# Kernel tuning notes

Measured on AMD Instinct MI355X. Metric: run time of the kernel, lower is better.

The kernel has to match this reference:

```python
import jax, jax.numpy as jnp
import numpy as np
import math

DIM = 256
PATCH = 16  # Patchnum
H = W = 64  # feature_size
B = 16


def _conv(x, w, pad):
    # x: [B,C,H,W], w: [O,I,kh,kw]
    return jax.lax.conv_general_dilated(
        x, w, window_strides=(1, 1), padding=[(pad, pad), (pad, pad)],
        dimension_numbers=('NCHW', 'OIHW', 'NCHW'))


def setup_inputs() -> dict:
    key = jax.random.key(0)
    ks = jax.random.split(key, 6)
    fan = DIM * 9
    s3 = 1.0 / math.sqrt(fan)
    s1 = 1.0 / math.sqrt(DIM)
    return {
        'e': jax.random.normal(ks[0], (B, DIM, H, W), dtype=jnp.float32),
        'pam_out': jax.random.normal(ks[1], (B, DIM, PATCH, PATCH), dtype=jnp.float32),
        'q_w': jax.random.uniform(ks[2], (DIM, DIM, 3, 3), jnp.float32, -s3, s3),
        'k_w': jax.random.uniform(ks[3], (DIM, DIM, 3, 3), jnp.float32, -s3, s3),
        'v_w': jax.random.uniform(ks[4], (DIM, DIM, 3, 3), jnp.float32, -s3, s3),
        'proj_w': jax.random.uniform(ks[5], (DIM, DIM, 1, 1), jnp.float32, -s1, s1),
    }


def reference(e, pam_out, q_w, k_w, v_w, proj_w):
    b, c, h, w = e.shape
    # AdaptiveAvgPool2d((PATCH, PATCH)) with h % PATCH == 0 -> mean pooling
    fh, fw = h // PATCH, w // PATCH
    max_e = e.reshape(b, c, PATCH, fh, PATCH, fw).mean(axis=(3, 5))
    q = _conv(max_e, q_w, 1).reshape(b, c, PATCH * PATCH)      # [b,c,P^2]
    k = _conv(pam_out, k_w, 1).reshape(b, c, PATCH * PATCH)    # [b,c,P^2]
    v = _conv(e, v_w, 1).reshape(b, c, h * w)                  # [b,c,HW]
    # L2 normalize along token dim (torch F.normalize, eps=1e-12)
    q = q / jnp.maximum(jnp.linalg.norm(q, axis=-1, keepdims=True), 1e-12)
    k = k / jnp.maximum(jnp.linalg.norm(k, axis=-1, keepdims=True), 1e-12)
    attn = jnp.einsum('bcn,bdn->bcd', q, k) / math.sqrt(c)     # [b,c,c]
    attn = jax.nn.softmax(attn, axis=-1)
    out = jnp.einsum('bcd,bdn->bcn', attn, v).reshape(b, c, h, w)
    out = _conv(out, proj_w, 0) + e
    return out
```

## Files before the change

kernel.cpp:

```cpp
#include <hip/hip_runtime.h>
#include <hip/hip_bf16.h>

#define NB 16
#define NC 256
#define NPIX 4096

typedef __attribute__((ext_vector_type(8))) short short8;
typedef __attribute__((ext_vector_type(4))) short short4v;
typedef __attribute__((ext_vector_type(4))) float f32x4;

static __device__ __forceinline__ ushort f2bf(float f) {
    __hip_bfloat16 h = __float2bfloat16(f);
    return *(ushort*)&h;
}

static __device__ __forceinline__ void gload_lds16(const ushort* g, ushort* l) {
    __builtin_amdgcn_global_load_lds(
        (const __attribute__((address_space(1))) unsigned int*)g,
        (__attribute__((address_space(3))) unsigned int*)l, 16, 0, 0);
}

__global__ void __launch_bounds__(256) prep_k(
    const float* __restrict__ e, const float* __restrict__ pam,
    const float* __restrict__ qw, const float* __restrict__ kw,
    const float* __restrict__ vw, const float* __restrict__ pw,
    ushort* __restrict__ et, ushort* __restrict__ maxeT, ushort* __restrict__ pamT,
    ushort* __restrict__ wqT, ushort* __restrict__ wkT,
    ushort* __restrict__ pbf, ushort* __restrict__ vwT,
    float* __restrict__ qnorm, float* __restrict__ knorm) {
    __shared__ float smem[9216];
    int blk = blockIdx.x, t = threadIdx.x;
    if (blk < 512) {
        int b = blk >> 5;
        int py = (blk >> 1) & 15;
        int xh = blk & 1;
        float (*lt)[32] = (float(*)[32])smem;
        float pool[8];
#pragma unroll
        for (int rr = 0; rr < 8; ++rr) pool[rr] = 0.f;
        int px = t & 7;
        int x4 = px * 4;
        int cg = t >> 3;
        for (int r = 0; r < 4; ++r) {
            int y = py * 4 + r;
            if (r) __syncthreads();
            const float* ep = e + (size_t)b * NC * NPIX + y * 64 + xh * 32;
#pragma unroll
            for (int rr = 0; rr < 8; ++rr) {
                int c = rr * 32 + cg;
                float4 v = *(const float4*)(ep + (size_t)c * NPIX + x4);
                pool[rr] += v.x + v.y + v.z + v.w;
                int s = (c >> 3) & 31;
                lt[c][(x4 + 0) ^ s] = v.x;
                lt[c][(x4 + 1) ^ s] = v.y;
                lt[c][(x4 + 2) ^ s] = v.z;
                lt[c][(x4 + 3) ^ s] = v.w;
            }
            __syncthreads();
            int l = t & 31, c0 = l * 8;
            ushort* op = et + ((size_t)((b * 64 + y) * 64) + xh * 32) * 256;
#pragma unroll
            for (int rx = 0; rx < 4; ++rx) {
                int x = rx * 8 + (t >> 5);
                short8 v;
#pragma unroll
                for (int k = 0; k < 8; ++k) v[k] = (short)f2bf(lt[c0 + k][x ^ l]);
                *(short8*)(op + (size_t)x * 256 + c0) = v;
            }
        }
        int tok = py * 16 + xh * 8 + px;
        ushort* md = maxeT + (size_t)b * 65536 + (size_t)tok * 256;
#pragma unroll
        for (int rr = 0; rr < 8; ++rr)
            md[rr * 32 + cg] = f2bf(pool[rr] * 0.0625f);
    } else if (blk < 768) {
        int bb = blk - 512;
        int b = bb >> 4, cg = bb & 15;
        float (*lt)[256] = (float(*)[256])smem;
#pragma unroll
        for (int cc = 0; cc < 16; ++cc)
            lt[cc][t] = pam[(size_t)(b * 256 + cg * 16 + cc) * 256 + t];
        __syncthreads();
        ushort* dstb = pamT + (size_t)b * 65536 + (size_t)t * 256 + cg * 16;
#pragma unroll
        for (int g = 0; g < 2; ++g) {
            short8 v;
#pragma unroll
            for (int k = 0; k < 8; ++k) v[k] = (short)f2bf(lt[g * 8 + k][t]);
            *(short8*)(dstb + g * 8) = v;
        }
    } else if (blk < 1280) {
        int idx = blk - 768;
        const float* src = (idx < 256) ? qw : kw;
        ushort* dst = (idx < 256) ? wqT : wkT;
        int o = idx & 255;
        float wv[9];
#pragma unroll
        for (int j = 0; j < 9; ++j) wv[j] = src[(size_t)o * 2304 + t * 9 + j];
#pragma unroll
        for (int j = 0; j < 9; ++j) dst[(size_t)j * 65536 + (size_t)o * 256 + t] = f2bf(wv[j]);
    } else if (blk < 1296) {
        int base = (blk - 1280) * 4096;
        for (int g = 0; g < 16; ++g) {
            int idx = base + g * 256 + t;
            pbf[idx] = f2bf(pw[idx]);
        }
    } else if (blk < 1360) {
        int d0 = (blk - 1296) * 4;
        float* lt = smem;
        for (int u = 0; u < 36; ++u) lt[u * 256 + t] = vw[(size_t)d0 * 2304 + u * 256 + t];
        __syncthreads();
#pragma unroll
        for (int r = 0; r < 9; ++r) {
            int idx = r * 256 + t;
            int i = idx / 9, j = idx % 9;
            short4v v;
#pragma unroll
            for (int dd = 0; dd < 4; ++dd) v[dd] = (short)f2bf(lt[dd * 2304 + idx]);
            *(short4v*)(vwT + ((size_t)(j * 256 + i)) * 256 + d0) = v;
        }
    } else {
        for (int g = 0; g < 16; ++g) {
            qnorm[g * 256 + t] = 0.f;
            knorm[g * 256 + t] = 0.f;
        }
    }
}

__global__ void __launch_bounds__(256, 2) conv16_mfma(const ushort* __restrict__ maxeT,
                                                      const ushort* __restrict__ pamT,
                                                      const ushort* __restrict__ wqT,
                                                      const ushort* __restrict__ wkT,
                                                      ushort* __restrict__ qb,
                                                      ushort* __restrict__ kTb,
                                                      float* __restrict__ qnorm,
                                                      float* __restrict__ knorm) {
    int blk = blockIdx.x;
    int qk = blk >> 8;
    int b  = (blk >> 4) & 15;
    int og = (blk >> 2) & 3;
    int tg = blk & 3;
    const ushort* inT = qk ? pamT : maxeT;
    const ushort* wt  = qk ? wkT : wqT;
    ushort* outp      = qk ? kTb : qb;
    float* nrm        = qk ? knorm : qnorm;
    int tid = threadIdx.x, wid = tid >> 6, lane = tid & 63;
    int wm = wid >> 1, wn = wid & 1;
    int kq = lane >> 4, l16 = lane & 15;
    int ty0 = tg * 4;
    __shared__ ushort Bs[96][256];
    __shared__ ushort As[2][64][128];
    const ushort* itb = inT + (size_t)b * 65536;
    {
#pragma unroll
        for (int j = 0; j < 12; ++j) {
            int d = (j * 4 + wid) * 64 + lane;
            int tok = d >> 5, u = d & 31;
            int lr = tok >> 4, tx = tok & 15;
            int gy = min(max(ty0 - 1 + lr, 0), 15);
            gload_lds16(itb + (gy * 16 + tx) * 256 + ((u ^ (tok & 7)) * 8),
                        &Bs[0][0] + (size_t)(j * 4 + wid) * 512);
        }
    }
    int aoff[4];
#pragma unroll
    for (int j = 0; j < 4; ++j) {
        int d = (j * 4 + wid) * 64 + lane;
        int o = d >> 4, u = d & 15;
        aoff[j] = (og * 64 + o) * 256 + ((u ^ (o & 7)) * 8);
    }
    auto stageA = [&](int s, int buf) {
        const ushort* base = wt + (size_t)(s >> 1) * 65536 + (s & 1) * 128;
#pragma unroll
        for (int j = 0; j < 4; ++j)
            gload_lds16(base + aoff[j], &As[buf][0][0] + (size_t)(j * 4 + wid) * 512);
    };
    stageA(0, 0);
    stageA(1, 1);
    __syncthreads();
    f32x4 acc[2][2];
#pragma unroll
    for (int mf = 0; mf < 2; ++mf)
#pragma unroll
        for (int nf = 0; nf < 2; ++nf) acc[mf][nf] = (f32x4){0.f, 0.f, 0.f, 0.f};
    const short8 zf = {};
#pragma unroll
    for (int s = 0; s < 18; ++s) {
        int tap = s >> 1, half = s & 1;
        int dy = tap / 3 - 1, dx = tap % 3 - 1;
        const ushort* bp[2]; bool ok[2]; int lt7[2];
#pragma unroll
        for (int nf = 0; nf < 2; ++nf) {
            int n = tg * 64 + wn * 32 + nf * 16 + l16;
            int ny = (n >> 4) + dy, nx = (n & 15) + dx;
            ok[nf] = ((unsigned)ny < 16u) && ((unsigned)nx < 16u);
            int lrc = min(max(ny - ty0 + 1, 0), 5);
            int nxc = min(max(nx, 0), 15);
            int ltok = lrc * 16 + nxc;
            bp[nf] = &Bs[ltok][0];
            lt7[nf] = ltok & 7;
        }
#pragma unroll
        for (int kc = 0; kc < 4; ++kc) {
            int ua = kc * 4 + kq;
            int ub = half * 16 + kc * 4 + kq;
            short8 af[2], bfr[2];
#pragma unroll
            for (int mf = 0; mf < 2; ++mf) {
                int o = wm * 32 + mf * 16 + l16;
                af[mf] = *(const short8*)(&As[s & 1][o][(ua ^ (o & 7)) * 8]);
            }
#pragma unroll
            for (int nf = 0; nf < 2; ++nf) {
                short8 v = *(const short8*)(bp[nf] + ((ub ^ lt7[nf]) * 8));
                bfr[nf] = ok[nf] ? v : zf;
            }
#pragma unroll
            for (int mf = 0; mf < 2; ++mf)
#pragma unroll
                for (int nf = 0; nf < 2; ++nf)
                    acc[mf][nf] = __builtin_amdgcn_mfma_f32_16x16x32_bf16(af[mf], bfr[nf], acc[mf][nf], 0, 0, 0);
        }
        __syncthreads();
        if (s + 2 < 18) stageA(s + 2, s & 1);
    }
    float ss[2][4];
#pragma unroll
    for (int mf = 0; mf < 2; ++mf)
#pragma unroll
        for (int r = 0; r < 4; ++r) ss[mf][r] = 0.f;
#pragma unroll
    for (int mf = 0; mf < 2; ++mf)
#pragma unroll
        for (int nf = 0; nf < 2; ++nf)
#pragma unroll
            for (int r = 0; r < 4; ++r) ss[mf][r] += acc[mf][nf][r] * acc[mf][nf][r];
#pragma unroll
    for (int mf = 0; mf < 2; ++mf)
#pragma unroll
        for (int r = 0; r < 4; ++r) {
#pragma unroll
            for (int off = 1; off < 16; off <<= 1) ss[mf][r] += __shfl_xor(ss[mf][r], off, 64);
        }
    if (l16 == 0) {
#pragma unroll
        for (int mf = 0; mf < 2; ++mf)
#pragma unroll
            for (int r = 0; r < 4; ++r)
                atomicAdd(&nrm[b * 256 + og * 64 + wm * 32 + mf * 16 + kq * 4 + r], ss[mf][r]);
    }
    ushort* ob = outp + (size_t)b * 65536;
#pragma unroll
    for (int mf = 0; mf < 2; ++mf)
#pragma unroll
        for (int nf = 0; nf < 2; ++nf) {
            int col = tg * 64 + wn * 32 + nf * 16 + l16;
#pragma unroll
            for (int r = 0; r < 4; ++r) {
                int row = og * 64 + wm * 32 + mf * 16 + kq * 4 + r;
                ob[(size_t)row * 256 + col] = f2bf(acc[mf][nf][r]);
            }
        }
}

__global__ void __launch_bounds__(512) attn_mfma(const ushort* __restrict__ qb,
                                                 const ushort* __restrict__ kTb,
                                                 const float* __restrict__ qnorm,
                                                 const float* __restrict__ knorm,
                                                 ushort* __restrict__ attnT) {
    int blk = blockIdx.x;
    int b = (blk & 7) + 8 * ((blk >> 3) & 1);
    int cg = blk >> 4;
    int tid = threadIdx.x, wid = tid >> 6, lane = tid & 63;
    int rw = wid & 1, chf = wid >> 1;
    int kq = lane >> 4, l16 = lane & 15;
    int c0w = cg * 32 + rw * 16;
    int lrow = rw * 16 + kq * 4;
    f32x4 acc[4];
#pragma unroll
    for (int nf = 0; nf < 4; ++nf) acc[nf] = (f32x4){0.f, 0.f, 0.f, 0.f};
    const ushort* qp = qb + (size_t)b * 65536;
    const ushort* kp = kTb + (size_t)b * 65536 + (size_t)(chf * 64) * 256;
    for (int kc = 0; kc < 8; ++kc) {
        short8 af = *(const short8*)(qp + (size_t)(c0w + l16) * 256 + kc * 32 + kq * 8);
#pragma unroll
        for (int nf = 0; nf < 4; ++nf) {
            short8 bf = *(const short8*)(kp + (size_t)(nf * 16 + l16) * 256 + kc * 32 + kq * 8);
            acc[nf] = __builtin_amdgcn_mfma_f32_16x16x32_bf16(af, bf, acc[nf], 0, 0, 0);
        }
    }
    float rq[4], rk[4];
#pragma unroll
    for (int r = 0; r < 4; ++r)
        rq[r] = rsqrtf(fmaxf(qnorm[b * 256 + c0w + kq * 4 + r], 1e-24f)) * 0.0625f;
#pragma unroll
    for (int nf = 0; nf < 4; ++nf)
        rk[nf] = rsqrtf(fmaxf(knorm[b * 256 + chf * 64 + nf * 16 + l16], 1e-24f));
#pragma unroll
    for (int nf = 0; nf < 4; ++nf)
#pragma unroll
        for (int r = 0; r < 4; ++r) acc[nf][r] *= rq[r] * rk[nf];
    __shared__ float red[32][4];
    float m4[4], s4[4];
#pragma unroll
    for (int r = 0; r < 4; ++r) {
        float m = -1e30f;
#pragma unroll
        for (int nf = 0; nf < 4; ++nf) m = fmaxf(m, acc[nf][r]);
#pragma unroll
        for (int off = 1; off < 16; off <<= 1) m = fmaxf(m, __shfl_xor(m, off, 64));
        m4[r] = m;
    }
    if (l16 == 0) {
#pragma unroll
        for (int r = 0; r < 4; ++r) red[lrow + r][chf] = m4[r];
    }
    __syncthreads();
#pragma unroll
    for (int r = 0; r < 4; ++r)
        m4[r] = fmaxf(fmaxf(red[lrow + r][0], red[lrow + r][1]),
                      fmaxf(red[lrow + r][2], red[lrow + r][3]));
    __syncthreads();
#pragma unroll
    for (int r = 0; r < 4; ++r) {
        float s = 0.f;
#pragma unroll
        for (int nf = 0; nf < 4; ++nf) {
            float ex = __expf(acc[nf][r] - m4[r]);
            acc[nf][r] = ex;
            s += ex;
        }
#pragma unroll
        for (int off = 1; off < 16; off <<= 1) s += __shfl_xor(s, off, 64);
        s4[r] = s;
    }
    if (l16 == 0) {
#pragma unroll
        for (int r = 0; r < 4; ++r) red[lrow + r][chf] = s4[r];
    }
    __syncthreads();
#pragma unroll
    for (int r = 0; r < 4; ++r) {
        float inv = 1.0f / (red[lrow + r][0] + red[lrow + r][1] +
                            red[lrow + r][2] + red[lrow + r][3]);
#pragma unroll
        for (int nf = 0; nf < 4; ++nf) acc[nf][r] *= inv;
    }
    ushort* ap = attnT + (size_t)b * 65536;
#pragma unroll
    for (int nf = 0; nf < 4; ++nf) {
        int d = chf * 64 + nf * 16 + l16;
        short4v v;
#pragma unroll
        for (int r = 0; r < 4; ++r) v[r] = (short)f2bf(acc[nf][r]);
        *(short4v*)(ap + (size_t)d * 256 + c0w + kq * 4) = v;
    }
}

__global__ void __launch_bounds__(512) mproj_mfma(const ushort* __restrict__ pbf,
                                                  const ushort* __restrict__ attnT,
                                                  ushort* __restrict__ Mbf) {
    int blk = blockIdx.x;
    int b = (blk & 7) + 8 * ((blk >> 3) & 1);
    int og = blk >> 4;
    int tid = threadIdx.x, wid = tid >> 6, lane = tid & 63;
    int rw = wid & 1, chf = wid >> 1;
    int kq = lane >> 4, l16 = lane & 15;
    int o0w = og * 32 + rw * 16;
    f32x4 acc[4];
#pragma unroll
    for (int nf = 0; nf < 4; ++nf) acc[nf] = (f32x4){0.f, 0.f, 0.f, 0.f};
    const ushort* ap = attnT + (size_t)b * 65536 + (size_t)(chf * 64) * 256;
    for (int kc = 0; kc < 8; ++kc) {
        short8 af = *(const short8*)(pbf + (size_t)(o0w + l16) * 256 + kc * 32 + kq * 8);
#pragma unroll
        for (int nf = 0; nf < 4; ++nf) {
            short8 bf = *(const short8*)(ap + (size_t)(nf * 16 + l16) * 256 + kc * 32 + kq * 8);
            acc[nf] = __builtin_amdgcn_mfma_f32_16x16x32_bf16(af, bf, acc[nf], 0, 0, 0);
        }
    }
    ushort* mb = Mbf + (size_t)b * 65536;
#pragma unroll
    for (int nf = 0; nf < 4; ++nf)
#pragma unroll
        for (int r = 0; r < 4; ++r)
            mb[(size_t)(o0w + kq * 4 + r) * 256 + chf * 64 + nf * 16 + l16] = f2bf(acc[nf][r]);
}

__global__ void __launch_bounds__(512) weff_mfma(const ushort* __restrict__ Mbf,
                                                 const ushort* __restrict__ vwT,
                                                 ushort* __restrict__ wbf) {
    int blk = blockIdx.x;
    int wg = (blk % 8) * 18 + blk / 8;
    int b = wg / 9, j = wg % 9;
    int tid = threadIdx.x;
    int wid = tid >> 6, lane = tid & 63;
    int wm = wid >> 1, wn = wid & 1;
    int kq = lane >> 4, l16 = lane & 15;
    f32x4 acc[4][8];
#pragma unroll
    for (int mf = 0; mf < 4; ++mf)
#pragma unroll
        for (int nf = 0; nf < 8; ++nf) acc[mf][nf] = (f32x4){0.f, 0.f, 0.f, 0.f};
    const ushort* abase = Mbf + (size_t)b * 65536 + (size_t)(wm * 64 + l16) * 256 + kq * 8;
    const ushort* bbase = vwT + (size_t)(j * 256 + wn * 128 + l16) * 256 + kq * 8;
    for (int kc = 0; kc < 8; ++kc) {
        int d0 = kc * 32;
        short8 af[4], bfr[8];
#pragma unroll
        for (int mf = 0; mf < 4; ++mf) af[mf] = *(const short8*)(abase + mf * 16 * 256 + d0);
#pragma unroll
        for (int nf = 0; nf < 8; ++nf) bfr[nf] = *(const short8*)(bbase + nf * 16 * 256 + d0);
#pragma unroll
        for (int mf = 0; mf < 4; ++mf)
#pragma unroll
            for (int nf = 0; nf < 8; ++nf)
                acc[mf][nf] = __builtin_amdgcn_mfma_f32_16x16x32_bf16(af[mf], bfr[nf], acc[mf][nf], 0, 0, 0);
    }
    ushort* wout = wbf + ((size_t)(b * 9 + j)) * 65536;
#pragma unroll
    for (int mf = 0; mf < 4; ++mf) {
        int o = wm * 64 + mf * 16 + kq * 4;
#pragma unroll
        for (int nf = 0; nf < 8; ++nf) {
            int ic = wn * 128 + nf * 16 + l16;
#pragma unroll
            for (int r = 0; r < 4; ++r)
                wout[(size_t)(o + r) * 256 + ic] = f2bf(acc[mf][nf][r]);
        }
    }
}

__global__ void __launch_bounds__(512, 4) bigconv_mfma(const ushort* __restrict__ et,
                                                       const ushort* __restrict__ wbf,
                                                       const float* __restrict__ e,
                                                       float* __restrict__ out) {
    int blk = blockIdx.x;
    int ibf = blk >> 3;
    int b = (blk & 7) + 8 * (ibf >> 5);
    int rem = ibf & 31;
    int pt = rem >> 1, oh = rem & 1;
    int y0 = pt * 4;
    int tid = threadIdx.x, wid = tid >> 6, lane = tid & 63;
    int wr = wid >> 1, wo = wid & 1;
    int kq = lane >> 4, l16 = lane & 15;
    __shared__ ushort Bs[6][64][64];
    __shared__ ushort As[2][128][64];
    f32x4 acc[4][4];
#pragma unroll
    for (int mf = 0; mf < 4; ++mf)
#pragma unroll
        for (int nf = 0; nf < 4; ++nf) acc[mf][nf] = (f32x4){0.f, 0.f, 0.f, 0.f};
    const ushort* etb = et + (size_t)b * 1048576;
    const float* eb = e + (size_t)b * NC * NPIX;
    const ushort* wb = wbf + (size_t)b * 589824;
    const short8 zf = {};
    int bpx = (tid >> 3) & 63, bu = tid & 7;
    int bsw = (bu ^ (bpx & 7)) * 8;
    int byc[6];
#pragma unroll
    for (int j = 0; j < 6; ++j) byc[j] = min(max(y0 - 1 + j, 0), 63);
    int ao[2], asd[2];
#pragma unroll
    for (int j = 0; j < 2; ++j) {
        int du = (j * 8 + wid) * 64 + lane;
        ao[j] = du >> 3;
        asd[j] = (du & 7) ^ (ao[j] & 7);
    }
    auto stageA = [&](int tap, int buf, int ci) {
        const ushort* base = wb + (size_t)tap * 65536 + ci * 64;
#pragma unroll
        for (int j = 0; j < 2; ++j)
            gload_lds16(base + (size_t)(oh * 128 + ao[j]) * 256 + asd[j] * 8,
                        &As[buf][0][0] + (size_t)(j * 8 + wid) * 512);
    };

    for (int ci = 0; ci < 4; ++ci) {
        {
#pragma unroll
            for (int j = 0; j < 6; ++j) {
                const ushort* src = etb + (((size_t)(byc[j] * 64 + bpx)) << 8) + ci * 64 + bsw;
                gload_lds16(src, &Bs[0][0][0] + (size_t)(j * 4096 + wid * 512));
            }
        }
        stageA(0, 0, ci);
        __syncthreads();
#pragma unroll
        for (int tap = 0; tap < 9; ++tap) {
            int cur = tap & 1;
            if (tap < 8) stageA(tap + 1, cur ^ 1, ci);
            {
                const int dy = tap / 3 - 1, dx = tap % 3 - 1;
                const int rl = wr + dy + 1;
                const bool rowok = (unsigned)(y0 + wr + dy) < 64u;
                const ushort* bp[4]; bool ok[4]; int p7[4];
#pragma unroll
                for (int nf = 0; nf < 4; ++nf) {
                    int pxr = nf * 16 + l16 + dx;
                    ok[nf] = rowok && ((unsigned)pxr < 64u);
                    int pxc = min(max(pxr, 0), 63);
                    bp[nf] = &Bs[rl][pxc][0];
                    p7[nf] = pxc & 7;
                }
#pragma unroll
                for (int kc = 0; kc < 2; ++kc) {
                    int sd = kc * 4 + kq;
                    short8 af[4];
#pragma unroll
                    for (int mf = 0; mf < 4; ++mf) {
                        int o = wo * 64 + mf * 16 + l16;
                        af[mf] = *(const short8*)(&As[cur][o][(sd ^ (o & 7)) * 8]);
                    }
                    short8 bfr[4];
#pragma unroll
                    for (int nf = 0; nf < 4; ++nf) {
                        short8 v = *(const short8*)(bp[nf] + (sd ^ p7[nf]) * 8);
                        bfr[nf] = ok[nf] ? v : zf;
                    }
                    __builtin_amdgcn_s_setprio(1);
#pragma unroll
                    for (int mf = 0; mf < 4; ++mf)
#pragma unroll
                        for (int nf = 0; nf < 4; ++nf)
                            acc[mf][nf] = __builtin_amdgcn_mfma_f32_16x16x32_bf16(af[mf], bfr[nf], acc[mf][nf], 0, 0, 0);
                    __builtin_amdgcn_s_setprio(0);
                }
            }
            __syncthreads();
        }
    }
    int prow = y0 + wr;
    float* ob = out + (size_t)b * NC * NPIX;
#pragma unroll
    for (int mf = 0; mf < 4; ++mf) {
        int o = oh * 128 + wo * 64 + mf * 16 + kq * 4;
#pragma unroll
        for (int nf = 0; nf < 4; ++nf) {
            int p = prow * 64 + nf * 16 + l16;
#pragma unroll
            for (int r = 0; r < 4; ++r) {
                size_t idx = (size_t)(o + r) * NPIX + p;
                ob[idx] = acc[mf][nf][r] + eb[idx];
            }
        }
    }
}

extern "C" void kernel_launch(void* const* d_in, const int* in_sizes, int n_in,
                              void* d_out, int out_size, void* d_ws, size_t ws_size,
                              hipStream_t stream) {
    const float* e   = (const float*)d_in[0];
    const float* pam = (const float*)d_in[1];
    const float* qw  = (const float*)d_in[2];
    const float* kw  = (const float*)d_in[3];
    const float* vw  = (const float*)d_in[4];
    const float* pw  = (const float*)d_in[5];
    float* out = (float*)d_out;
    float* ws  = (float*)d_ws;

    ushort* et   = (ushort*)ws;
    ushort* wbf  = (ushort*)(ws + 8388608);
    float*  S    = ws + 13107200;
    ushort* maxeT = (ushort*)S;
    ushort* pamT  = (ushort*)(S + 524288);
    ushort* wqT   = (ushort*)(S + 1048576);
    ushort* wkT   = (ushort*)(S + 1343488);
    ushort* pbf   = (ushort*)(S + 1638400);
    ushort* vwT   = (ushort*)(S + 1671168);
    float*  qnorm = S + 1966080;
    float*  knorm = S + 1970176;
    ushort* qb    = (ushort*)(ws + 8388608);
    ushort* kTb   = (ushort*)(ws + 8912896);
    ushort* attnT = maxeT;
    ushort* Mbf   = pamT;

    prep_k<<<1361, 256, 0, stream>>>(e, pam, qw, kw, vw, pw,
                                     et, maxeT, pamT, wqT, wkT, pbf, vwT, qnorm, knorm);
    conv16_mfma<<<512, 256, 0, stream>>>(maxeT, pamT, wqT, wkT, qb, kTb, qnorm, knorm);
    attn_mfma<<<128, 512, 0, stream>>>(qb, kTb, qnorm, knorm, attnT);
    mproj_mfma<<<128, 512, 0, stream>>>(pbf, attnT, Mbf);
    weff_mfma<<<144, 512, 0, stream>>>(Mbf, vwT, wbf);
    bigconv_mfma<<<512, 512, 0, stream>>>(et, wbf, e, out);
}
```

Baseline: 171.7 us.

## Halve bigconv block to 4 waves, each computing a 64x128 output tile

The final fused conv kernel now runs 256 threads (4 waves) instead of 8. Each wave covers two output rows, so it holds 4x8 MFMA accumulators instead of 4x4. Each A-fragment LDS read now feeds twice as many MFMAs, and each thread issues more of the staging loads. The cost is roughly double the accumulator registers, lower occupancy (launch bounds 256,2) and fewer waves available to hide latency.

```diff
diff --git a/kernel.cpp b/kernel.cpp
--- a/kernel.cpp
+++ b/kernel.cpp
@@ -431,7 +431,7 @@
     }
 }
 
-__global__ void __launch_bounds__(512, 4) bigconv_mfma(const ushort* __restrict__ et,
+__global__ void __launch_bounds__(256, 2) bigconv_mfma(const ushort* __restrict__ et,
                                                        const ushort* __restrict__ wbf,
                                                        const float* __restrict__ e,
                                                        float* __restrict__ out) {
@@ -442,46 +442,50 @@
     int pt = rem >> 1, oh = rem & 1;
     int y0 = pt * 4;
     int tid = threadIdx.x, wid = tid >> 6, lane = tid & 63;
-    int wr = wid >> 1, wo = wid & 1;
+    int wy = wid >> 1, wo = wid & 1;
     int kq = lane >> 4, l16 = lane & 15;
     __shared__ ushort Bs[6][64][64];
     __shared__ ushort As[2][128][64];
-    f32x4 acc[4][4];
+    f32x4 acc[4][8];
 #pragma unroll
     for (int mf = 0; mf < 4; ++mf)
 #pragma unroll
-        for (int nf = 0; nf < 4; ++nf) acc[mf][nf] = (f32x4){0.f, 0.f, 0.f, 0.f};
+        for (int nf = 0; nf < 8; ++nf) acc[mf][nf] = (f32x4){0.f, 0.f, 0.f, 0.f};
     const ushort* etb = et + (size_t)b * 1048576;
     const float* eb = e + (size_t)b * NC * NPIX;
     const ushort* wb = wbf + (size_t)b * 589824;
     const short8 zf = {};
-    int bpx = (tid >> 3) & 63, bu = tid & 7;
-    int bsw = (bu ^ (bpx & 7)) * 8;
-    int byc[6];
-#pragma unroll
-    for (int j = 0; j < 6; ++j) byc[j] = min(max(y0 - 1 + j, 0), 63);
-    int ao[2], asd[2];
-#pragma unroll
-    for (int j = 0; j < 2; ++j) {
-        int du = (j * 8 + wid) * 64 + lane;
-        ao[j] = du >> 3;
-        asd[j] = (du & 7) ^ (ao[j] & 7);
+    int boff[12];
+#pragma unroll
+    for (int j = 0; j < 12; ++j) {
+        int c = j * 4 + wid;
+        int row = c >> 3, sub = c & 7;
+        int px = sub * 8 + (lane >> 3);
+        int u = lane & 7;
+        int yc = min(max(y0 - 1 + row, 0), 63);
+        boff[j] = ((yc * 64 + px) << 8) + ((u ^ (px & 7)) * 8);
+    }
+    int aoff[4];
+#pragma unroll
+    for (int j = 0; j < 4; ++j) {
+        int c = j * 4 + wid;
+        int o = c * 8 + (lane >> 3);
+        int u = lane & 7;
+        aoff[j] = (size_t)0 + (oh * 128 + o) * 256 + ((u ^ (o & 7)) * 8);
     }
     auto stageA = [&](int tap, int buf, int ci) {
         const ushort* base = wb + (size_t)tap * 65536 + ci * 64;
 #pragma unroll
-        for (int j = 0; j < 2; ++j)
-            gload_lds16(base + (size_t)(oh * 128 + ao[j]) * 256 + asd[j] * 8,
-                        &As[buf][0][0] + (size_t)(j * 8 + wid) * 512);
+        for (int j = 0; j < 4; ++j)
+            gload_lds16(base + aoff[j], &As[buf][0][0] + (size_t)(j * 4 + wid) * 512);
     };
 
     for (int ci = 0; ci < 4; ++ci) {
         {
 #pragma unroll
-            for (int j = 0; j < 6; ++j) {
-                const ushort* src = etb + (((size_t)(byc[j] * 64 + bpx)) << 8) + ci * 64 + bsw;
-                gload_lds16(src, &Bs[0][0][0] + (size_t)(j * 4096 + wid * 512));
-            }
+            for (int j = 0; j < 12; ++j)
+                gload_lds16(etb + boff[j] + ci * 64,
+                            &Bs[0][0][0] + (size_t)(j * 4 + wid) * 512);
         }
         stageA(0, 0, ci);
         __syncthreads();
@@ -491,13 +495,14 @@
             if (tap < 8) stageA(tap + 1, cur ^ 1, ci);
             {
                 const int dy = tap / 3 - 1, dx = tap % 3 - 1;
-                const int rl = wr + dy + 1;
-                const bool rowok = (unsigned)(y0 + wr + dy) < 64u;
-                const ushort* bp[4]; bool ok[4]; int p7[4];
-#pragma unroll
-                for (int nf = 0; nf < 4; ++nf) {
-                    int pxr = nf * 16 + l16 + dx;
-                    ok[nf] = rowok && ((unsigned)pxr < 64u);
+                const ushort* bp[8]; bool ok[8]; int p7[8];
+#pragma unroll
+                for (int nf = 0; nf < 8; ++nf) {
+                    int h = nf >> 2;
+                    int yabs = y0 + wy * 2 + h + dy;
+                    int rl = wy * 2 + h + dy + 1;
+                    int pxr = (nf & 3) * 16 + l16 + dx;
+                    ok[nf] = ((unsigned)yabs < 64u) && ((unsigned)pxr < 64u);
                     int pxc = min(max(pxr, 0), 63);
                     bp[nf] = &Bs[rl][pxc][0];
                     p7[nf] = pxc & 7;
@@ -511,9 +516,9 @@
                         int o = wo * 64 + mf * 16 + l16;
                         af[mf] = *(const short8*)(&As[cur][o][(sd ^ (o & 7)) * 8]);
                     }
-                    short8 bfr[4];
-#pragma unroll
-                    for (int nf = 0; nf < 4; ++nf) {
+                    short8 bfr[8];
+#pragma unroll
+                    for (int nf = 0; nf < 8; ++nf) {
                         short8 v = *(const short8*)(bp[nf] + (sd ^ p7[nf]) * 8);
                         bfr[nf] = ok[nf] ? v : zf;
                     }
@@ -521,7 +526,7 @@
 #pragma unroll
                     for (int mf = 0; mf < 4; ++mf)
 #pragma unroll
-                        for (int nf = 0; nf < 4; ++nf)
+                        for (int nf = 0; nf < 8; ++nf)
                             acc[mf][nf] = __builtin_amdgcn_mfma_f32_16x16x32_bf16(af[mf], bfr[nf], acc[mf][nf], 0, 0, 0);
                     __builtin_amdgcn_s_setprio(0);
                 }
@@ -529,14 +534,14 @@
             __syncthreads();
         }
     }
-    int prow = y0 + wr;
     float* ob = out + (size_t)b * NC * NPIX;
 #pragma unroll
     for (int mf = 0; mf < 4; ++mf) {
         int o = oh * 128 + wo * 64 + mf * 16 + kq * 4;
 #pragma unroll
-        for (int nf = 0; nf < 4; ++nf) {
-            int p = prow * 64 + nf * 16 + l16;
+        for (int nf = 0; nf < 8; ++nf) {
+            int y = y0 + wy * 2 + (nf >> 2);
+            int p = y * 64 + (nf & 3) * 16 + l16;
 #pragma unroll
             for (int r = 0; r < 4; ++r) {
                 size_t idx = (size_t)(o + r) * NPIX + p;
@@ -580,5 +585,5 @@
     attn_mfma<<<128, 512, 0, stream>>>(qb, kTb, qnorm, knorm, attnT);
     mproj_mfma<<<128, 512, 0, stream>>>(pbf, attnT, Mbf);
     weff_mfma<<<144, 512, 0, stream>>>(Mbf, vwT, wbf);
-    bigconv_mfma<<<512, 512, 0, stream>>>(et, wbf, e, out);
-}
+    bigconv_mfma<<<512, 256, 0, stream>>>(et, wbf, e, out);
+}
```

Result: no change. 172.0 us (+0.2%).

## Halve K-chunk and triple-buffer weight taps with explicit vmcnt waits

Applied to the files above, without the earlier changes.

Cuts the channel chunk per stage from 64 to 32, which halves the B and A LDS tiles and doubles the outer ci loop. Weight tiles are now triple-buffered and prefetched two taps ahead, and __syncthreads is replaced by manual s_waitcnt vmcnt plus s_barrier so loads can overlap MFMA work. The smaller LDS footprint may allow more resident blocks. In exchange there are twice as many B-tile reloads and barriers, and the result depends on the hand-counted vmcnt values being correct.

```diff
diff --git a/kernel.cpp b/kernel.cpp
--- a/kernel.cpp
+++ b/kernel.cpp
@@ -444,8 +444,8 @@
     int tid = threadIdx.x, wid = tid >> 6, lane = tid & 63;
     int wr = wid >> 1, wo = wid & 1;
     int kq = lane >> 4, l16 = lane & 15;
-    __shared__ ushort Bs[6][64][64];
-    __shared__ ushort As[2][128][64];
+    __shared__ ushort Bs[6][64][32];
+    __shared__ ushort As[3][128][32];
     f32x4 acc[4][4];
 #pragma unroll
     for (int mf = 0; mf < 4; ++mf)
@@ -455,78 +455,80 @@
     const float* eb = e + (size_t)b * NC * NPIX;
     const ushort* wb = wbf + (size_t)b * 589824;
     const short8 zf = {};
-    int bpx = (tid >> 3) & 63, bu = tid & 7;
-    int bsw = (bu ^ (bpx & 7)) * 8;
-    int byc[6];
-#pragma unroll
-    for (int j = 0; j < 6; ++j) byc[j] = min(max(y0 - 1 + j, 0), 63);
-    int ao[2], asd[2];
-#pragma unroll
-    for (int j = 0; j < 2; ++j) {
-        int du = (j * 8 + wid) * 64 + lane;
-        ao[j] = du >> 3;
-        asd[j] = (du & 7) ^ (ao[j] & 7);
+    int boff[3];
+#pragma unroll
+    for (int j = 0; j < 3; ++j) {
+        int idx = j * 512 + tid;
+        int row = idx >> 8;
+        int px = (idx >> 2) & 63;
+        int u = idx & 3;
+        int yc = min(max(y0 - 1 + row, 0), 63);
+        boff[j] = ((yc * 64 + px) << 8) + ((u ^ ((px >> 1) & 3)) * 8);
+    }
+    int ao_;
+    {
+        int o = tid >> 2, u = tid & 3;
+        ao_ = (oh * 128 + o) * 256 + ((u ^ ((o >> 1) & 3)) * 8);
     }
     auto stageA = [&](int tap, int buf, int ci) {
-        const ushort* base = wb + (size_t)tap * 65536 + ci * 64;
-#pragma unroll
-        for (int j = 0; j < 2; ++j)
-            gload_lds16(base + (size_t)(oh * 128 + ao[j]) * 256 + asd[j] * 8,
-                        &As[buf][0][0] + (size_t)(j * 8 + wid) * 512);
+        gload_lds16(wb + (size_t)tap * 65536 + ci * 32 + ao_,
+                    &As[buf][0][0] + (size_t)tid * 8);
     };
 
-    for (int ci = 0; ci < 4; ++ci) {
-        {
-#pragma unroll
-            for (int j = 0; j < 6; ++j) {
-                const ushort* src = etb + (((size_t)(byc[j] * 64 + bpx)) << 8) + ci * 64 + bsw;
-                gload_lds16(src, &Bs[0][0][0] + (size_t)(j * 4096 + wid * 512));
-            }
-        }
+    for (int ci = 0; ci < 8; ++ci) {
+#pragma unroll
+        for (int j = 0; j < 3; ++j)
+            gload_lds16(etb + boff[j] + ci * 32,
+                        &Bs[0][0][0] + (size_t)(j * 512 + tid) * 8);
         stageA(0, 0, ci);
-        __syncthreads();
+        stageA(1, 1, ci);
+        asm volatile("s_waitcnt vmcnt(1)" ::: "memory");
+        __builtin_amdgcn_sched_barrier(0);
+        __builtin_amdgcn_s_barrier();
 #pragma unroll
         for (int tap = 0; tap < 9; ++tap) {
-            int cur = tap & 1;
-            if (tap < 8) stageA(tap + 1, cur ^ 1, ci);
+            int cur = tap % 3;
             {
                 const int dy = tap / 3 - 1, dx = tap % 3 - 1;
                 const int rl = wr + dy + 1;
                 const bool rowok = (unsigned)(y0 + wr + dy) < 64u;
-                const ushort* bp[4]; bool ok[4]; int p7[4];
+                const ushort* bp[4]; bool ok[4]; int p3[4];
 #pragma unroll
                 for (int nf = 0; nf < 4; ++nf) {
                     int pxr = nf * 16 + l16 + dx;
                     ok[nf] = rowok && ((unsigned)pxr < 64u);
                     int pxc = min(max(pxr, 0), 63);
                     bp[nf] = &Bs[rl][pxc][0];
-                    p7[nf] = pxc & 7;
+                    p3[nf] = (pxc >> 1) & 3;
                 }
-#pragma unroll
-                for (int kc = 0; kc < 2; ++kc) {
-                    int sd = kc * 4 + kq;
-                    short8 af[4];
-#pragma unroll
-                    for (int mf = 0; mf < 4; ++mf) {
-                        int o = wo * 64 + mf * 16 + l16;
-                        af[mf] = *(const short8*)(&As[cur][o][(sd ^ (o & 7)) * 8]);
-                    }
-                    short8 bfr[4];
-#pragma unroll
-                    for (int nf = 0; nf < 4; ++nf) {
-                        short8 v = *(const short8*)(bp[nf] + (sd ^ p7[nf]) * 8);
-                        bfr[nf] = ok[nf] ? v : zf;
-                    }
-                    __builtin_amdgcn_s_setprio(1);
-#pragma unroll
-                    for (int mf = 0; mf < 4; ++mf)
-#pragma unroll
-                        for (int nf = 0; nf < 4; ++nf)
-                            acc[mf][nf] = __builtin_amdgcn_mfma_f32_16x16x32_bf16(af[mf], bfr[nf], acc[mf][nf], 0, 0, 0);
-                    __builtin_amdgcn_s_setprio(0);
+                short8 af[4];
+#pragma unroll
+                for (int mf = 0; mf < 4; ++mf) {
+                    int o = wo * 64 + mf * 16 + l16;
+                    af[mf] = *(const short8*)(&As[cur][o][(kq ^ ((o >> 1) & 3)) * 8]);
                 }
-            }
-            __syncthreads();
+                short8 bfr[4];
+#pragma unroll
+                for (int nf = 0; nf < 4; ++nf) {
+                    short8 v = *(const short8*)(bp[nf] + ((kq ^ p3[nf]) * 8));
+                    bfr[nf] = ok[nf] ? v : zf;
+                }
+                __builtin_amdgcn_s_setprio(1);
+#pragma unroll
+                for (int mf = 0; mf < 4; ++mf)
+#pragma unroll
+                    for (int nf = 0; nf < 4; ++nf)
+                        acc[mf][nf] = __builtin_amdgcn_mfma_f32_16x16x32_bf16(af[mf], bfr[nf], acc[mf][nf], 0, 0, 0);
+                __builtin_amdgcn_s_setprio(0);
+            }
+            if (tap + 2 < 9) stageA(tap + 2, (tap + 2) % 3, ci);
+            if (tap < 7) {
+                asm volatile("s_waitcnt vmcnt(1)" ::: "memory");
+            } else {
+                asm volatile("s_waitcnt vmcnt(0)" ::: "memory");
+            }
+            __builtin_amdgcn_sched_barrier(0);
+            __builtin_amdgcn_s_barrier();
         }
     }
     int prow = y0 + wr;
```

Result: no change. 173.9 us (+1.3%).
